# Optimization experiments

Hardware: AMD Instinct MI355X
Metric: run time of the kernel (lower is better)

The kernel has to match this reference:

```python
import jax, jax.numpy as jnp
import numpy as np

L = 10      # LSTM layers
H = 128     # hidden size
ENC = 4096  # traffic_encoder_output_len
B = 8192    # batch
T = 12      # points_to_predict
NUM_MODES = 25


def setup_inputs() -> dict:
    key = jax.random.key(0)
    ks = jax.random.split(key, 10)
    s = 1.0 / np.sqrt(H)
    return {
        "backbone_encoded": jax.random.normal(ks[0], (B, ENC), jnp.float32),
        "fc_in_W": jax.random.normal(ks[1], (H, ENC), jnp.float32) / np.sqrt(ENC),
        "fc_in_b": jax.random.normal(ks[2], (H,), jnp.float32) * s,
        "Wih": jax.random.normal(ks[3], (L, 4 * H, H), jnp.float32) * s,
        "Whh": jax.random.normal(ks[4], (L, 4 * H, H), jnp.float32) * s,
        "bih": jax.random.normal(ks[5], (L, 4 * H), jnp.float32) * s,
        "bhh": jax.random.normal(ks[6], (L, 4 * H), jnp.float32) * s,
        "fc_out_W": jax.random.normal(ks[7], (3 * NUM_MODES, H), jnp.float32) * s,
        "fc_out_b": jax.random.normal(ks[8], (3 * NUM_MODES,), jnp.float32) * s,
        "points_to_predict": T,
    }


def _lstm_stack(x, Wih, Whh, bih, bhh):
    # x: [B, T, H]; PyTorch gate order: i, f, g, o
    def run_layer(x, l):
        def step(carry, xt):
            h, c = carry
            gates = xt @ Wih[l].T + h @ Whh[l].T + bih[l] + bhh[l]  # [B, 4H]
            i, f, g, o = jnp.split(gates, 4, axis=-1)
            c = jax.nn.sigmoid(f) * c + jax.nn.sigmoid(i) * jnp.tanh(g)
            h = jax.nn.sigmoid(o) * jnp.tanh(c)
            return (h, c), h
        b = x.shape[0]
        h0 = jnp.zeros((b, H), x.dtype)
        _, ys = jax.lax.scan(step, (h0, h0), jnp.swapaxes(x, 0, 1))  # [T, B, H]
        return jnp.swapaxes(ys, 0, 1)

    for l in range(L):
        x = run_layer(x, l)
    return x


def reference(backbone_encoded, fc_in_W, fc_in_b, Wih, Whh, bih, bhh,
              fc_out_W, fc_out_b, points_to_predict):
    enc = jax.nn.relu(backbone_encoded @ fc_in_W.T + fc_in_b)        # [B, H]
    x = jnp.repeat(enc[:, None, :], points_to_predict, axis=1)      # [B, T, H]
    y = _lstm_stack(x, Wih, Whh, bih, bhh)                           # [B, T, H]
    fc = y @ fc_out_W.T + fc_out_b                                   # [B, T, 75]
    b, t, _ = fc.shape
    # chunk(25, dim=channels) of consecutive pairs -> [B, 25, T, 2]
    predictions = fc[:, :, :50].reshape(b, t, NUM_MODES, 2).transpose(0, 2, 1, 3)
    probabilities = jax.nn.softmax(fc[:, -1, 50:], axis=-1)          # [B, 25]
    return predictions, probabilities
```

## Files before the change

### kernel.cpp

```cpp
#include <hip/hip_runtime.h>

typedef _Float16 h16;
typedef _Float16 h4 __attribute__((ext_vector_type(4)));
typedef _Float16 h8 __attribute__((ext_vector_type(8)));
typedef float f4 __attribute__((ext_vector_type(4)));

#define NB 8192
#define NENC 4096
#define NH 128
#define NL 10
#define NT 12
#define PAD 136
#define L2E 1.4426950408889634f
#define K2 -2.8853900817779268f

#define OFF_FCIN 0
#define SZ_FCIN (128*4096)
#define OFF_W (OFF_FCIN + SZ_FCIN)
#define SZ_W (10*2*512*128)
#define OFF_FCOUT (OFF_W + SZ_W)
#define SZ_FCOUT (80*128)
#define OFF_ENC (OFF_FCOUT + SZ_FCOUT)
#define SZ_ENC (8192*128)
#define OFF_GX0 (OFF_ENC + SZ_ENC)
#define SZ_GX0 (8192*512)
#define BYTE_BIAS ((OFF_GX0 + SZ_GX0)*2)

__device__ __forceinline__ f4 splat4(float v) { f4 r; r[0]=v; r[1]=v; r[2]=v; r[3]=v; return r; }
__device__ __forceinline__ h8 cvt8(float4 a, float4 b) {
  h8 r; r[0]=(h16)a.x; r[1]=(h16)a.y; r[2]=(h16)a.z; r[3]=(h16)a.w;
  r[4]=(h16)b.x; r[5]=(h16)b.y; r[6]=(h16)b.z; r[7]=(h16)b.w; return r;
}
__device__ __forceinline__ h8 cvt8s(float4 a, float4 b, float sc) {
  h8 r; r[0]=(h16)(a.x*sc); r[1]=(h16)(a.y*sc); r[2]=(h16)(a.z*sc); r[3]=(h16)(a.w*sc);
  r[4]=(h16)(b.x*sc); r[5]=(h16)(b.y*sc); r[6]=(h16)(b.z*sc); r[7]=(h16)(b.w*sc); return r;
}

__device__ __forceinline__ h16 cell(float iv, float fv, float gv, float ov, float& c) {
  float ei = __builtin_amdgcn_exp2f(iv);
  float ef = __builtin_amdgcn_exp2f(fv);
  float eg = __builtin_amdgcn_exp2f(gv);
  float eo = __builtin_amdgcn_exp2f(ov);
  float ai = 1.f + ei, af = 1.f + ef, ag = 1.f + eg;
  float m1 = ai * ag;
  float R1 = __builtin_amdgcn_rcpf(af * m1);
  float cc = R1 * fmaf(af, 1.f - eg, c * m1);
  c = cc;
  float ec = __builtin_amdgcn_exp2f(K2 * cc);
  float R2 = __builtin_amdgcn_rcpf((1.f + eo) * (1.f + ec));
  return (h16)(R2 * (1.f - ec));
}

__global__ __launch_bounds__(256) void prep(const float* __restrict__ fcinW,
                                            const float* __restrict__ Wih,
                                            const float* __restrict__ Whh,
                                            const float* __restrict__ bih,
                                            const float* __restrict__ bhh,
                                            const float* __restrict__ fcoutW,
                                            h16* __restrict__ wsh,
                                            float* __restrict__ wbias) {
  int idx = blockIdx.x * 256 + threadIdx.x;
  if (idx < 65536) {
    int r = idx >> 9, k8 = idx & 511;
    const float* src = fcinW + r * 4096 + k8 * 8;
    h8 v = cvt8(*(const float4*)src, *(const float4*)(src + 4));
    *(h8*)(wsh + OFF_FCIN + (((r >> 4) * 512 + k8) * 128 + (r & 15) * 8)) = v;
  } else if (idx < 229376) {
    int rel = idx - 65536;
    int l = rel >> 14, rr = rel & 16383;
    int ssel = rr >> 13, rk8 = rr & 8191;
    int r = rk8 >> 4, k8 = rk8 & 15;
    float sc = ((r >> 7) == 2) ? (-2.f * L2E) : (-L2E);
    const float* src = (ssel ? Whh : Wih) + l * 65536 + r * 128 + k8 * 8;
    h8 v = cvt8s(*(const float4*)src, *(const float4*)(src + 4), sc);
    *(h8*)(wsh + OFF_W + (l * 2 + ssel) * 65536 +
           (((r >> 4) * 16 + k8) * 128 + (r & 15) * 8)) = v;
  } else if (idx < 230656) {
    int rel = idx - 229376;
    int r = rel >> 4, k8 = rel & 15;
    h8 v;
    if (r < 75) {
      const float* src = fcoutW + r * 128 + k8 * 8;
      v = cvt8(*(const float4*)src, *(const float4*)(src + 4));
    } else {
      for (int j = 0; j < 8; ++j) v[j] = (h16)0.f;
    }
    *(h8*)(wsh + OFF_FCOUT + (((r >> 4) * 16 + k8) * 128 + (r & 15) * 8)) = v;
  } else if (idx < 235776) {
    int rel = idx - 230656;
    int col = rel & 511;
    float sc = ((col >> 7) == 2) ? (-2.f * L2E) : (-L2E);
    wbias[rel] = (bih[rel] + bhh[rel]) * sc;
  }
}

__global__ __launch_bounds__(256) void kin(const float* __restrict__ A,
                                           const float* __restrict__ bvec,
                                           h16* __restrict__ wsh) {
  const h16* Wp = wsh + OFF_FCIN;
  h16* ench = wsh + OFF_ENC;
  int tid = threadIdx.x;
  int w = tid >> 6, lane = tid & 63, s = lane & 15, q = lane >> 4;
  int m0 = blockIdx.x * 16;
  int c0 = w * 32 + s, c1 = c0 + 16;
  f4 acc0 = splat4(bvec[c0]);
  f4 acc1 = splat4(bvec[c1]);
  const float* arow = A + (size_t)(m0 + s) * NENC;
  const h16* wp0 = Wp + (w * 2 + 0) * (512 * 128) + s * 8;
  const h16* wp1 = Wp + (w * 2 + 1) * (512 * 128) + s * 8;
#pragma unroll 4
  for (int kb = 0; kb < 128; ++kb) {
    int k0 = kb * 32 + q * 8;
    float4 x0 = *(const float4*)(arow + k0);
    float4 x1 = *(const float4*)(arow + k0 + 4);
    h8 af = cvt8(x0, x1);
    h8 b0 = *(const h8*)(wp0 + (kb * 4 + q) * 128);
    h8 b1 = *(const h8*)(wp1 + (kb * 4 + q) * 128);
    acc0 = __builtin_amdgcn_mfma_f32_16x16x32_f16(af, b0, acc0, 0, 0, 0);
    acc1 = __builtin_amdgcn_mfma_f32_16x16x32_f16(af, b1, acc1, 0, 0, 0);
  }
#pragma unroll
  for (int r = 0; r < 4; ++r) {
    int b = m0 + q * 4 + r;
    float v0 = acc0[r]; v0 = v0 > 0.f ? v0 : 0.f;
    float v1 = acc1[r]; v1 = v1 > 0.f ? v1 : 0.f;
    ench[(size_t)b * NH + c0] = (h16)v0;
    ench[(size_t)b * NH + c1] = (h16)v1;
  }
}

__global__ __launch_bounds__(256) void kin2(h16* __restrict__ wsh,
                                            const float* __restrict__ wbias) {
  int tid = threadIdx.x;
  int w2 = tid >> 6, lane = tid & 63, s = lane & 15, q = lane >> 4;
  int bid = blockIdx.x;
  int lb = bid >> 3, mt = (bid >> 2) & 1, cg = bid & 3;
  const h16* ench = wsh + OFF_ENC;
  const h16* wih0 = wsh + OFF_W;
  h16* gx0 = wsh + OFF_GX0;
  const h16* arow = ench + (size_t)(lb * 32 + mt * 16 + s) * NH;
  h8 ax[4];
#pragma unroll
  for (int kt = 0; kt < 4; ++kt) ax[kt] = *(const h8*)(arow + kt * 32 + q * 8);
#pragma unroll
  for (int ti = 0; ti < 2; ++ti) {
    int W = w2 * 2 + ti;
    int rb = cg * 8 + W;
    f4 acc = splat4(wbias[cg * 128 + W * 16 + s]);
#pragma unroll
    for (int kt = 0; kt < 4; ++kt) {
      h8 b = *(const h8*)(wih0 + (rb * 16 + kt * 4 + q) * 128 + s * 8);
      acc = __builtin_amdgcn_mfma_f32_16x16x32_f16(ax[kt], b, acc, 0, 0, 0);
    }
    h4 st; st[0] = (h16)acc[0]; st[1] = (h16)acc[1]; st[2] = (h16)acc[2]; st[3] = (h16)acc[3];
    *(h4*)(gx0 + ((((size_t)lb * 8 + W) * 8 + cg * 2 + mt) * 64 + lane) * 4) = st;
  }
}

__global__ __launch_bounds__(512, 2) void lstm(h16* __restrict__ wsh,
                                               const float* __restrict__ wbias,
                                               const float* __restrict__ fcoutb,
                                               float* __restrict__ out) {
  __shared__ h16 ring[32][13][PAD];
  __shared__ float probst[32 * 26];
  int tid = threadIdx.x;
  int w = tid >> 6, lane = tid & 63, s = lane & 15, q = lane >> 4;
  int brow = blockIdx.x * 32;
  h8 wx[4][4], wh[4][4];
  f4 bbv[4];
  float c[2][4];
  h16* rd0 = &ring[s][0][q * 8];
  h16* rd1 = &ring[16 + s][0][q * 8];
  h16* wr0 = &ring[q * 4][0][w * 16 + s];
  h16* wr1 = &ring[16 + q * 4][0][w * 16 + s];
#define RSTRIDE (13 * PAD)

  {
    const h16* whh = wsh + OFF_W + 65536;
#pragma unroll
    for (int g = 0; g < 4; ++g)
#pragma unroll
      for (int kt = 0; kt < 4; ++kt)
        wh[g][kt] = *(const h8*)(whh + (((g * 8 + w) * 16 + kt * 4 + q) * 128) + s * 8);
    f4 gx[4][2];
    const h16* gxp = wsh + OFF_GX0 + ((size_t)blockIdx.x * 8 + w) * 8 * 256 + (size_t)lane * 4;
#pragma unroll
    for (int g = 0; g < 4; ++g)
#pragma unroll
      for (int mt = 0; mt < 2; ++mt) {
        h4 v = *(const h4*)(gxp + (g * 2 + mt) * 256);
        f4 a; a[0] = (float)v[0]; a[1] = (float)v[1]; a[2] = (float)v[2]; a[3] = (float)v[3];
        gx[g][mt] = a;
      }
#pragma unroll
    for (int mt = 0; mt < 2; ++mt)
#pragma unroll
      for (int r = 0; r < 4; ++r) c[mt][r] = 0.f;
    {
      h16* q0 = wr0 + 11 * PAD;
      h16* q1 = wr1 + 11 * PAD;
#pragma unroll
      for (int mt = 0; mt < 2; ++mt) {
        h16* qq = mt ? q1 : q0;
#pragma unroll
        for (int r = 0; r < 4; ++r)
          qq[r * RSTRIDE] = cell(gx[0][mt][r], gx[1][mt][r], gx[2][mt][r], gx[3][mt][r], c[mt][r]);
      }
    }
    int rw = 12;
    for (int t = 1; t < NT; ++t) {
      __syncthreads();
      int rh = rw - 1; if (rh < 0) rh += 13;
      f4 acc[4][2];
      const h16* p0 = rd0 + rh * PAD;
      const h16* p1 = rd1 + rh * PAD;
#pragma unroll
      for (int mt = 0; mt < 2; ++mt) {
        const h16* pp = mt ? p1 : p0;
        h8 ah[4];
#pragma unroll
        for (int kt = 0; kt < 4; ++kt) ah[kt] = *(const h8*)(pp + kt * 32);
#pragma unroll
        for (int g = 0; g < 4; ++g) {
          acc[g][mt] = __builtin_amdgcn_mfma_f32_16x16x32_f16(ah[0], wh[g][0], gx[g][mt], 0, 0, 0);
#pragma unroll
          for (int kt = 1; kt < 4; ++kt)
            acc[g][mt] = __builtin_amdgcn_mfma_f32_16x16x32_f16(ah[kt], wh[g][kt], acc[g][mt], 0, 0, 0);
        }
      }
      h16* q0 = wr0 + rw * PAD;
      h16* q1 = wr1 + rw * PAD;
#pragma unroll
      for (int mt = 0; mt < 2; ++mt) {
        h16* qq = mt ? q1 : q0;
#pragma unroll
        for (int r = 0; r < 4; ++r)
          qq[r * RSTRIDE] = cell(acc[0][mt][r], acc[1][mt][r], acc[2][mt][r], acc[3][mt][r], c[mt][r]);
      }
      ++rw; if (rw >= 13) rw = 0;
    }
  }
  for (int l = 1; l < NL; ++l) {
    const h16* wih = wsh + OFF_W + (size_t)(l * 2) * 65536;
    const h16* whh = wih + 65536;
#pragma unroll
    for (int g = 0; g < 4; ++g) {
#pragma unroll
      for (int kt = 0; kt < 4; ++kt) {
        int off = (((g * 8 + w) * 16 + kt * 4 + q) * 128) + s * 8;
        wx[g][kt] = *(const h8*)(wih + off);
        wh[g][kt] = *(const h8*)(whh + off);
      }
      bbv[g] = splat4(wbias[l * 512 + g * 128 + w * 16 + s]);
    }
#pragma unroll
    for (int mt = 0; mt < 2; ++mt)
#pragma unroll
      for (int r = 0; r < 4; ++r) c[mt][r] = 0.f;
    int rw = 11 - l;
    f4 acc[4][2];
    {
      const h16* p0 = rd0 + (rw + 1) * PAD;
      const h16* p1 = rd1 + (rw + 1) * PAD;
#pragma unroll
      for (int mt = 0; mt < 2; ++mt) {
        const h16* pp = mt ? p1 : p0;
        h8 ax[4];
#pragma unroll
        for (int kt = 0; kt < 4; ++kt) ax[kt] = *(const h8*)(pp + kt * 32);
#pragma unroll
        for (int g = 0; g < 4; ++g) {
          acc[g][mt] = __builtin_amdgcn_mfma_f32_16x16x32_f16(ax[0], wx[g][0], bbv[g], 0, 0, 0);
#pragma unroll
          for (int kt = 1; kt < 4; ++kt)
            acc[g][mt] = __builtin_amdgcn_mfma_f32_16x16x32_f16(ax[kt], wx[g][kt], acc[g][mt], 0, 0, 0);
        }
      }
    }
    for (int t = 0; t < NT; ++t) {
      __syncthreads();
      if (t > 0) {
        int rh = rw - 1; if (rh < 0) rh += 13;
        const h16* p0 = rd0 + rh * PAD;
        const h16* p1 = rd1 + rh * PAD;
#pragma unroll
        for (int mt = 0; mt < 2; ++mt) {
          const h16* pp = mt ? p1 : p0;
          h8 ah[4];
#pragma unroll
          for (int kt = 0; kt < 4; ++kt) ah[kt] = *(const h8*)(pp + kt * 32);
#pragma unroll
          for (int g = 0; g < 4; ++g)
#pragma unroll
            for (int kt = 0; kt < 4; ++kt)
              acc[g][mt] = __builtin_amdgcn_mfma_f32_16x16x32_f16(ah[kt], wh[g][kt], acc[g][mt], 0, 0, 0);
        }
      }
      h16 hv[2][4];
#pragma unroll
      for (int mt = 0; mt < 2; ++mt)
#pragma unroll
        for (int r = 0; r < 4; ++r)
          hv[mt][r] = cell(acc[0][mt][r], acc[1][mt][r], acc[2][mt][r], acc[3][mt][r], c[mt][r]);
      if (t < 11) {
        int rx = rw + 2; if (rx >= 13) rx -= 13;
        const h16* p0 = rd0 + rx * PAD;
        const h16* p1 = rd1 + rx * PAD;
#pragma unroll
        for (int mt = 0; mt < 2; ++mt) {
          const h16* pp = mt ? p1 : p0;
          h8 ax[4];
#pragma unroll
          for (int kt = 0; kt < 4; ++kt) ax[kt] = *(const h8*)(pp + kt * 32);
#pragma unroll
          for (int g = 0; g < 4; ++g) {
            acc[g][mt] = __builtin_amdgcn_mfma_f32_16x16x32_f16(ax[0], wx[g][0], bbv[g], 0, 0, 0);
#pragma unroll
            for (int kt = 1; kt < 4; ++kt)
              acc[g][mt] = __builtin_amdgcn_mfma_f32_16x16x32_f16(ax[kt], wx[g][kt], acc[g][mt], 0, 0, 0);
          }
        }
      }
      h16* q0 = wr0 + rw * PAD;
      h16* q1 = wr1 + rw * PAD;
#pragma unroll
      for (int mt = 0; mt < 2; ++mt) {
        h16* qq = mt ? q1 : q0;
#pragma unroll
        for (int r = 0; r < 4; ++r) qq[r * RSTRIDE] = hv[mt][r];
      }
      ++rw; if (rw >= 13) rw = 0;
    }
  }
  __syncthreads();
  h8 wo[5][4];
  float bo[5];
  const h16* fco = wsh + OFF_FCOUT;
#pragma unroll
  for (int nt = 0; nt < 5; ++nt) {
#pragma unroll
    for (int kt = 0; kt < 4; ++kt)
      wo[nt][kt] = *(const h8*)(fco + (nt * 16 + kt * 4 + q) * 128 + s * 8);
    int col = nt * 16 + s;
    bo[nt] = (col < 75) ? fcoutb[col] : 0.f;
  }
  int tcount = (w < 4) ? 2 : 1;
  for (int ti = 0; ti < tcount; ++ti) {
    int t = w + ti * 8;
    int sl = t + 2; if (sl >= 13) sl -= 13;
#pragma unroll
    for (int mt = 0; mt < 2; ++mt) {
      const h16* pp = (mt ? rd1 : rd0) + sl * PAD;
      h8 ax[4];
#pragma unroll
      for (int kt = 0; kt < 4; ++kt) ax[kt] = *(const h8*)(pp + kt * 32);
#pragma unroll
      for (int nt = 0; nt < 5; ++nt) {
        f4 a = splat4(bo[nt]);
#pragma unroll
        for (int kt = 0; kt < 4; ++kt)
          a = __builtin_amdgcn_mfma_f32_16x16x32_f16(ax[kt], wo[nt][kt], a, 0, 0, 0);
        int col = nt * 16 + s;
#pragma unroll
        for (int r = 0; r < 4; ++r) {
          int row = mt * 16 + q * 4 + r;
          int b = brow + row;
          float v = a[r];
          if (col < 50)
            out[(size_t)b * 600 + (col >> 1) * 24 + t * 2 + (col & 1)] = v;
          if (t == 11 && col >= 50 && col < 75)
            probst[row * 26 + (col - 50)] = v;
        }
      }
    }
  }
  __syncthreads();
  if (tid < 32) {
    float vals[25];
    float m = -1e30f;
#pragma unroll
    for (int j = 0; j < 25; ++j) { vals[j] = probst[tid * 26 + j]; m = vals[j] > m ? vals[j] : m; }
    float sum = 0.f;
#pragma unroll
    for (int j = 0; j < 25; ++j) {
      float e = __builtin_amdgcn_exp2f((vals[j] - m) * L2E);
      vals[j] = e; sum += e;
    }
    float rs = 1.0f / sum;
    size_t pb = (size_t)4915200 + (size_t)(brow + tid) * 25;
#pragma unroll
    for (int j = 0; j < 25; ++j) out[pb + j] = vals[j] * rs;
  }
}

extern "C" void kernel_launch(void* const* d_in, const int* in_sizes, int n_in,
                              void* d_out, int out_size, void* d_ws, size_t ws_size,
                              hipStream_t stream) {
  const float* backbone = (const float*)d_in[0];
  const float* fcinW    = (const float*)d_in[1];
  const float* fcinb    = (const float*)d_in[2];
  const float* Wih      = (const float*)d_in[3];
  const float* Whh      = (const float*)d_in[4];
  const float* bih      = (const float*)d_in[5];
  const float* bhh      = (const float*)d_in[6];
  const float* fcoutW   = (const float*)d_in[7];
  const float* fcoutb   = (const float*)d_in[8];
  h16* wsh = (h16*)d_ws;
  float* wbias = (float*)((char*)d_ws + BYTE_BIAS);

  prep<<<922, 256, 0, stream>>>(fcinW, Wih, Whh, bih, bhh, fcoutW, wsh, wbias);
  kin<<<512, 256, 0, stream>>>(backbone, fcinb, wsh);
  kin2<<<2048, 256, 0, stream>>>(wsh, wbias);
  lstm<<<256, 512, 0, stream>>>(wsh, wbias, fcoutb, (float*)d_out);
}
```

Baseline: 494.1 us.

## Split fc_in K across waves with LDS reduction and prefetch LSTM inputs

The input projection kernel now has each of the four waves cover a quarter of the 4096-long K dimension for all 128 output columns, instead of a slice of columns over the full K. The partial sums are reduced through shared memory before bias and ReLU, so each wave reads its own portion of the activation row rather than every wave streaming the whole row. In the LSTM wavefront loop, the next step's x-operand fragments are loaded from LDS one step early and the h outputs are written straight to LDS, to hide load latency. The cost is a 33KB shared buffer, a block barrier, and more live registers (eight accumulators, and the prefetched fragments held across the step).

```diff
diff --git a/kernel.cpp b/kernel.cpp
--- a/kernel.cpp
+++ b/kernel.cpp
@@ -97,35 +97,43 @@
 __global__ __launch_bounds__(256) void kin(const float* __restrict__ A,
                                            const float* __restrict__ bvec,
                                            h16* __restrict__ wsh) {
+  __shared__ float red[4][16][129];
   const h16* Wp = wsh + OFF_FCIN;
   h16* ench = wsh + OFF_ENC;
   int tid = threadIdx.x;
   int w = tid >> 6, lane = tid & 63, s = lane & 15, q = lane >> 4;
   int m0 = blockIdx.x * 16;
-  int c0 = w * 32 + s, c1 = c0 + 16;
-  f4 acc0 = splat4(bvec[c0]);
-  f4 acc1 = splat4(bvec[c1]);
-  const float* arow = A + (size_t)(m0 + s) * NENC;
-  const h16* wp0 = Wp + (w * 2 + 0) * (512 * 128) + s * 8;
-  const h16* wp1 = Wp + (w * 2 + 1) * (512 * 128) + s * 8;
+  f4 acc[8];
+#pragma unroll
+  for (int ct = 0; ct < 8; ++ct) acc[ct] = splat4(0.f);
+  const float* arow = A + (size_t)(m0 + s) * NENC + w * 1024;
+  const h16* wpk = Wp + ((size_t)(w * 128 + q)) * 128 + s * 8;
 #pragma unroll 4
-  for (int kb = 0; kb < 128; ++kb) {
+  for (int kb = 0; kb < 32; ++kb) {
     int k0 = kb * 32 + q * 8;
     float4 x0 = *(const float4*)(arow + k0);
     float4 x1 = *(const float4*)(arow + k0 + 4);
     h8 af = cvt8(x0, x1);
-    h8 b0 = *(const h8*)(wp0 + (kb * 4 + q) * 128);
-    h8 b1 = *(const h8*)(wp1 + (kb * 4 + q) * 128);
-    acc0 = __builtin_amdgcn_mfma_f32_16x16x32_f16(af, b0, acc0, 0, 0, 0);
-    acc1 = __builtin_amdgcn_mfma_f32_16x16x32_f16(af, b1, acc1, 0, 0, 0);
-  }
-#pragma unroll
-  for (int r = 0; r < 4; ++r) {
-    int b = m0 + q * 4 + r;
-    float v0 = acc0[r]; v0 = v0 > 0.f ? v0 : 0.f;
-    float v1 = acc1[r]; v1 = v1 > 0.f ? v1 : 0.f;
-    ench[(size_t)b * NH + c0] = (h16)v0;
-    ench[(size_t)b * NH + c1] = (h16)v1;
+#pragma unroll
+    for (int ct = 0; ct < 8; ++ct) {
+      h8 b = *(const h8*)(wpk + ((size_t)ct * 512 + kb * 4) * 128);
+      acc[ct] = __builtin_amdgcn_mfma_f32_16x16x32_f16(af, b, acc[ct], 0, 0, 0);
+    }
+  }
+#pragma unroll
+  for (int ct = 0; ct < 8; ++ct)
+#pragma unroll
+    for (int r = 0; r < 4; ++r)
+      red[w][q * 4 + r][ct * 16 + s] = acc[ct][r];
+  __syncthreads();
+#pragma unroll
+  for (int i = 0; i < 8; ++i) {
+    int idx = tid + i * 256;
+    int row = idx >> 7, col = idx & 127;
+    float v = red[0][row][col] + red[1][row][col] + red[2][row][col] + red[3][row][col]
+            + bvec[col];
+    v = v > 0.f ? v : 0.f;
+    ench[(size_t)(m0 + row) * NH + col] = (h16)v;
   }
 }
 
@@ -259,22 +267,32 @@
       for (int r = 0; r < 4; ++r) c[mt][r] = 0.f;
     int rw = 11 - l;
     f4 acc[4][2];
+    h8 ax[2][4];
     {
       const h16* p0 = rd0 + (rw + 1) * PAD;
       const h16* p1 = rd1 + (rw + 1) * PAD;
 #pragma unroll
       for (int mt = 0; mt < 2; ++mt) {
         const h16* pp = mt ? p1 : p0;
-        h8 ax[4];
-#pragma unroll
-        for (int kt = 0; kt < 4; ++kt) ax[kt] = *(const h8*)(pp + kt * 32);
+#pragma unroll
+        for (int kt = 0; kt < 4; ++kt) ax[mt][kt] = *(const h8*)(pp + kt * 32);
+      }
+#pragma unroll
+      for (int mt = 0; mt < 2; ++mt)
 #pragma unroll
         for (int g = 0; g < 4; ++g) {
-          acc[g][mt] = __builtin_amdgcn_mfma_f32_16x16x32_f16(ax[0], wx[g][0], bbv[g], 0, 0, 0);
+          acc[g][mt] = __builtin_amdgcn_mfma_f32_16x16x32_f16(ax[mt][0], wx[g][0], bbv[g], 0, 0, 0);
 #pragma unroll
           for (int kt = 1; kt < 4; ++kt)
-            acc[g][mt] = __builtin_amdgcn_mfma_f32_16x16x32_f16(ax[kt], wx[g][kt], acc[g][mt], 0, 0, 0);
+            acc[g][mt] = __builtin_amdgcn_mfma_f32_16x16x32_f16(ax[mt][kt], wx[g][kt], acc[g][mt], 0, 0, 0);
         }
+      const h16* n0 = rd0 + (rw + 2) * PAD;
+      const h16* n1 = rd1 + (rw + 2) * PAD;
+#pragma unroll
+      for (int mt = 0; mt < 2; ++mt) {
+        const h16* pp = mt ? n1 : n0;
+#pragma unroll
+        for (int kt = 0; kt < 4; ++kt) ax[mt][kt] = *(const h8*)(pp + kt * 32);
       }
     }
     for (int t = 0; t < NT; ++t) {
@@ -296,38 +314,36 @@
               acc[g][mt] = __builtin_amdgcn_mfma_f32_16x16x32_f16(ah[kt], wh[g][kt], acc[g][mt], 0, 0, 0);
         }
       }
-      h16 hv[2][4];
-#pragma unroll
-      for (int mt = 0; mt < 2; ++mt)
+      h16* q0 = wr0 + rw * PAD;
+      h16* q1 = wr1 + rw * PAD;
+#pragma unroll
+      for (int mt = 0; mt < 2; ++mt) {
+        h16* qq = mt ? q1 : q0;
 #pragma unroll
         for (int r = 0; r < 4; ++r)
-          hv[mt][r] = cell(acc[0][mt][r], acc[1][mt][r], acc[2][mt][r], acc[3][mt][r], c[mt][r]);
+          qq[r * RSTRIDE] = cell(acc[0][mt][r], acc[1][mt][r], acc[2][mt][r], acc[3][mt][r], c[mt][r]);
+      }
       if (t < 11) {
-        int rx = rw + 2; if (rx >= 13) rx -= 13;
-        const h16* p0 = rd0 + rx * PAD;
-        const h16* p1 = rd1 + rx * PAD;
-#pragma unroll
-        for (int mt = 0; mt < 2; ++mt) {
-          const h16* pp = mt ? p1 : p0;
-          h8 ax[4];
-#pragma unroll
-          for (int kt = 0; kt < 4; ++kt) ax[kt] = *(const h8*)(pp + kt * 32);
+#pragma unroll
+        for (int mt = 0; mt < 2; ++mt)
 #pragma unroll
           for (int g = 0; g < 4; ++g) {
-            acc[g][mt] = __builtin_amdgcn_mfma_f32_16x16x32_f16(ax[0], wx[g][0], bbv[g], 0, 0, 0);
+            acc[g][mt] = __builtin_amdgcn_mfma_f32_16x16x32_f16(ax[mt][0], wx[g][0], bbv[g], 0, 0, 0);
 #pragma unroll
             for (int kt = 1; kt < 4; ++kt)
-              acc[g][mt] = __builtin_amdgcn_mfma_f32_16x16x32_f16(ax[kt], wx[g][kt], acc[g][mt], 0, 0, 0);
+              acc[g][mt] = __builtin_amdgcn_mfma_f32_16x16x32_f16(ax[mt][kt], wx[g][kt], acc[g][mt], 0, 0, 0);
+          }
+        if (t < 10) {
+          int rx = rw + 3; if (rx >= 13) rx -= 13;
+          const h16* n0 = rd0 + rx * PAD;
+          const h16* n1 = rd1 + rx * PAD;
+#pragma unroll
+          for (int mt = 0; mt < 2; ++mt) {
+            const h16* pp = mt ? n1 : n0;
+#pragma unroll
+            for (int kt = 0; kt < 4; ++kt) ax[mt][kt] = *(const h8*)(pp + kt * 32);
           }
         }
-      }
-      h16* q0 = wr0 + rw * PAD;
-      h16* q1 = wr1 + rw * PAD;
-#pragma unroll
-      for (int mt = 0; mt < 2; ++mt) {
-        h16* qq = mt ? q1 : q0;
-#pragma unroll
-        for (int r = 0; r < 4; ++r) qq[r * RSTRIDE] = hv[mt][r];
       }
       ++rw; if (rw >= 13) rw = 0;
     }
```

New measurement: 532.9 us. 1.08x slower.

## Split fc_in K-dimension across waves with LDS reduction; vectorize LSTM cell math

Applied to the files above, without the earlier changes.

The fc_in GEMM kernel now has each of the four waves cover a quarter of the 4096-long K dimension for all 128 output columns, instead of each wave covering 32 columns over the full K. Each A fragment is thus converted once and reused across eight MFMAs, and the per-wave loop is four times shorter. The partial sums are reduced through a shared-memory buffer before bias, ReLU and the fp16 store. Separately, the LSTM cell nonlinearity is rewritten on 4-wide float vectors so the compiler can use packed float ops. The first part adds about 33 KB of LDS per block and a barrier.

```diff
diff --git a/kernel.cpp b/kernel.cpp
--- a/kernel.cpp
+++ b/kernel.cpp
@@ -36,19 +36,28 @@
   r[4]=(h16)(b.x*sc); r[5]=(h16)(b.y*sc); r[6]=(h16)(b.z*sc); r[7]=(h16)(b.w*sc); return r;
 }
 
-__device__ __forceinline__ h16 cell(float iv, float fv, float gv, float ov, float& c) {
-  float ei = __builtin_amdgcn_exp2f(iv);
-  float ef = __builtin_amdgcn_exp2f(fv);
-  float eg = __builtin_amdgcn_exp2f(gv);
-  float eo = __builtin_amdgcn_exp2f(ov);
-  float ai = 1.f + ei, af = 1.f + ef, ag = 1.f + eg;
-  float m1 = ai * ag;
-  float R1 = __builtin_amdgcn_rcpf(af * m1);
-  float cc = R1 * fmaf(af, 1.f - eg, c * m1);
+__device__ __forceinline__ f4 exp2v(f4 x) {
+  f4 r; r[0]=__builtin_amdgcn_exp2f(x[0]); r[1]=__builtin_amdgcn_exp2f(x[1]);
+  r[2]=__builtin_amdgcn_exp2f(x[2]); r[3]=__builtin_amdgcn_exp2f(x[3]); return r;
+}
+__device__ __forceinline__ f4 rcpv(f4 x) {
+  f4 r; r[0]=__builtin_amdgcn_rcpf(x[0]); r[1]=__builtin_amdgcn_rcpf(x[1]);
+  r[2]=__builtin_amdgcn_rcpf(x[2]); r[3]=__builtin_amdgcn_rcpf(x[3]); return r;
+}
+
+__device__ __forceinline__ h4 cell4(f4 iv, f4 fv, f4 gv, f4 ov, f4& c) {
+  f4 ei = exp2v(iv), ef = exp2v(fv), eg = exp2v(gv), eo = exp2v(ov);
+  f4 one = splat4(1.f);
+  f4 ai = one + ei, af = one + ef, ag = one + eg, ao = one + eo;
+  f4 m1 = ai * ag;
+  f4 R1 = rcpv(af * m1);
+  f4 cc = R1 * (af * (one - eg) + c * m1);
   c = cc;
-  float ec = __builtin_amdgcn_exp2f(K2 * cc);
-  float R2 = __builtin_amdgcn_rcpf((1.f + eo) * (1.f + ec));
-  return (h16)(R2 * (1.f - ec));
+  f4 ec = exp2v(splat4(K2) * cc);
+  f4 R2 = rcpv(ao * (one + ec));
+  f4 hv = R2 * (one - ec);
+  h4 o; o[0]=(h16)hv[0]; o[1]=(h16)hv[1]; o[2]=(h16)hv[2]; o[3]=(h16)hv[3];
+  return o;
 }
 
 __global__ __launch_bounds__(256) void prep(const float* __restrict__ fcinW,
@@ -97,35 +106,43 @@
 __global__ __launch_bounds__(256) void kin(const float* __restrict__ A,
                                            const float* __restrict__ bvec,
                                            h16* __restrict__ wsh) {
+  __shared__ float red[4][16][129];
   const h16* Wp = wsh + OFF_FCIN;
   h16* ench = wsh + OFF_ENC;
   int tid = threadIdx.x;
   int w = tid >> 6, lane = tid & 63, s = lane & 15, q = lane >> 4;
   int m0 = blockIdx.x * 16;
-  int c0 = w * 32 + s, c1 = c0 + 16;
-  f4 acc0 = splat4(bvec[c0]);
-  f4 acc1 = splat4(bvec[c1]);
-  const float* arow = A + (size_t)(m0 + s) * NENC;
-  const h16* wp0 = Wp + (w * 2 + 0) * (512 * 128) + s * 8;
-  const h16* wp1 = Wp + (w * 2 + 1) * (512 * 128) + s * 8;
+  f4 acc[8];
+#pragma unroll
+  for (int ct = 0; ct < 8; ++ct) acc[ct] = splat4(0.f);
+  const float* arow = A + (size_t)(m0 + s) * NENC + w * 1024;
+  const h16* wpk = Wp + ((size_t)(w * 128 + q)) * 128 + s * 8;
 #pragma unroll 4
-  for (int kb = 0; kb < 128; ++kb) {
+  for (int kb = 0; kb < 32; ++kb) {
     int k0 = kb * 32 + q * 8;
     float4 x0 = *(const float4*)(arow + k0);
     float4 x1 = *(const float4*)(arow + k0 + 4);
     h8 af = cvt8(x0, x1);
-    h8 b0 = *(const h8*)(wp0 + (kb * 4 + q) * 128);
-    h8 b1 = *(const h8*)(wp1 + (kb * 4 + q) * 128);
-    acc0 = __builtin_amdgcn_mfma_f32_16x16x32_f16(af, b0, acc0, 0, 0, 0);
-    acc1 = __builtin_amdgcn_mfma_f32_16x16x32_f16(af, b1, acc1, 0, 0, 0);
-  }
-#pragma unroll
-  for (int r = 0; r < 4; ++r) {
-    int b = m0 + q * 4 + r;
-    float v0 = acc0[r]; v0 = v0 > 0.f ? v0 : 0.f;
-    float v1 = acc1[r]; v1 = v1 > 0.f ? v1 : 0.f;
-    ench[(size_t)b * NH + c0] = (h16)v0;
-    ench[(size_t)b * NH + c1] = (h16)v1;
+#pragma unroll
+    for (int ct = 0; ct < 8; ++ct) {
+      h8 b = *(const h8*)(wpk + ((size_t)ct * 512 + kb * 4) * 128);
+      acc[ct] = __builtin_amdgcn_mfma_f32_16x16x32_f16(af, b, acc[ct], 0, 0, 0);
+    }
+  }
+#pragma unroll
+  for (int ct = 0; ct < 8; ++ct)
+#pragma unroll
+    for (int r = 0; r < 4; ++r)
+      red[w][q * 4 + r][ct * 16 + s] = acc[ct][r];
+  __syncthreads();
+#pragma unroll
+  for (int i = 0; i < 8; ++i) {
+    int idx = tid + i * 256;
+    int row = idx >> 7, col = idx & 127;
+    float v = red[0][row][col] + red[1][row][col] + red[2][row][col] + red[3][row][col]
+            + bvec[col];
+    v = v > 0.f ? v : 0.f;
+    ench[(size_t)(m0 + row) * NH + col] = (h16)v;
   }
 }
 
@@ -168,7 +185,7 @@
   int brow = blockIdx.x * 32;
   h8 wx[4][4], wh[4][4];
   f4 bbv[4];
-  float c[2][4];
+  f4 c[2];
   h16* rd0 = &ring[s][0][q * 8];
   h16* rd1 = &ring[16 + s][0][q * 8];
   h16* wr0 = &ring[q * 4][0][w * 16 + s];
@@ -192,20 +209,14 @@
         f4 a; a[0] = (float)v[0]; a[1] = (float)v[1]; a[2] = (float)v[2]; a[3] = (float)v[3];
         gx[g][mt] = a;
       }
-#pragma unroll
-    for (int mt = 0; mt < 2; ++mt)
-#pragma unroll
-      for (int r = 0; r < 4; ++r) c[mt][r] = 0.f;
+    c[0] = splat4(0.f); c[1] = splat4(0.f);
     {
       h16* q0 = wr0 + 11 * PAD;
       h16* q1 = wr1 + 11 * PAD;
-#pragma unroll
-      for (int mt = 0; mt < 2; ++mt) {
-        h16* qq = mt ? q1 : q0;
-#pragma unroll
-        for (int r = 0; r < 4; ++r)
-          qq[r * RSTRIDE] = cell(gx[0][mt][r], gx[1][mt][r], gx[2][mt][r], gx[3][mt][r], c[mt][r]);
-      }
+      h4 h0 = cell4(gx[0][0], gx[1][0], gx[2][0], gx[3][0], c[0]);
+      h4 h1 = cell4(gx[0][1], gx[1][1], gx[2][1], gx[3][1], c[1]);
+#pragma unroll
+      for (int r = 0; r < 4; ++r) { q0[r * RSTRIDE] = h0[r]; q1[r * RSTRIDE] = h1[r]; }
     }
     int rw = 12;
     for (int t = 1; t < NT; ++t) {
@@ -230,13 +241,10 @@
       }
       h16* q0 = wr0 + rw * PAD;
       h16* q1 = wr1 + rw * PAD;
-#pragma unroll
-      for (int mt = 0; mt < 2; ++mt) {
-        h16* qq = mt ? q1 : q0;
-#pragma unroll
-        for (int r = 0; r < 4; ++r)
-          qq[r * RSTRIDE] = cell(acc[0][mt][r], acc[1][mt][r], acc[2][mt][r], acc[3][mt][r], c[mt][r]);
-      }
+      h4 h0 = cell4(acc[0][0], acc[1][0], acc[2][0], acc[3][0], c[0]);
+      h4 h1 = cell4(acc[0][1], acc[1][1], acc[2][1], acc[3][1], c[1]);
+#pragma unroll
+      for (int r = 0; r < 4; ++r) { q0[r * RSTRIDE] = h0[r]; q1[r * RSTRIDE] = h1[r]; }
       ++rw; if (rw >= 13) rw = 0;
     }
   }
@@ -253,10 +261,7 @@
       }
       bbv[g] = splat4(wbias[l * 512 + g * 128 + w * 16 + s]);
     }
-#pragma unroll
-    for (int mt = 0; mt < 2; ++mt)
-#pragma unroll
-      for (int r = 0; r < 4; ++r) c[mt][r] = 0.f;
+    c[0] = splat4(0.f); c[1] = splat4(0.f);
     int rw = 11 - l;
     f4 acc[4][2];
     {
@@ -296,12 +301,8 @@
               acc[g][mt] = __builtin_amdgcn_mfma_f32_16x16x32_f16(ah[kt], wh[g][kt], acc[g][mt], 0, 0, 0);
         }
       }
-      h16 hv[2][4];
-#pragma unroll
-      for (int mt = 0; mt < 2; ++mt)
-#pragma unroll
-        for (int r = 0; r < 4; ++r)
-          hv[mt][r] = cell(acc[0][mt][r], acc[1][mt][r], acc[2][mt][r], acc[3][mt][r], c[mt][r]);
+      h4 h0 = cell4(acc[0][0], acc[1][0], acc[2][0], acc[3][0], c[0]);
+      h4 h1 = cell4(acc[0][1], acc[1][1], acc[2][1], acc[3][1], c[1]);
       if (t < 11) {
         int rx = rw + 2; if (rx >= 13) rx -= 13;
         const h16* p0 = rd0 + rx * PAD;
@@ -324,11 +325,7 @@
       h16* q0 = wr0 + rw * PAD;
       h16* q1 = wr1 + rw * PAD;
 #pragma unroll
-      for (int mt = 0; mt < 2; ++mt) {
-        h16* qq = mt ? q1 : q0;
-#pragma unroll
-        for (int r = 0; r < 4; ++r) qq[r * RSTRIDE] = hv[mt][r];
-      }
+      for (int r = 0; r < 4; ++r) { q0[r * RSTRIDE] = h0[r]; q1[r * RSTRIDE] = h1[r]; }
       ++rw; if (rw >= 13) rw = 0;
     }
   }
```

New measurement: 509.3 us. 1.03x slower.
